# Performance work log

Measured on AMD Instinct MI355X. Metric: run time of the kernel, lower is better.

The kernel has to match this reference:

```python
import jax, jax.numpy as jnp
import numpy as np

B, N, NP, NS = 4, 8192, 2048, 32
CIN, COUT = 128, 256
RADIUS = 0.2
RELU_ALPHA = 0.2
BN_EPS = 1e-5


def setup_inputs() -> dict:
    key = jax.random.key(0)
    k1, k2, k3, k4, k5, k6, k7 = jax.random.split(key, 7)
    xyz = jax.random.uniform(k1, (B, N, 3), dtype=jnp.float32)          # points in unit cube
    feats = jax.random.normal(k2, (B, CIN, N), dtype=jnp.float32)
    conv_w = jax.random.normal(k3, (COUT, CIN), dtype=jnp.float32) * 0.05  # 1x1 conv kernel (bias off: bn=True)
    gamma = jax.random.uniform(k4, (COUT,), minval=0.5, maxval=1.5)
    beta = jax.random.normal(k5, (COUT,)) * 0.1
    rmean = jax.random.normal(k6, (COUT,)) * 0.1                        # BN running mean (eval mode)
    rvar = jax.random.uniform(k7, (COUT,), minval=0.5, maxval=1.5)      # BN running var
    return dict(xyz=xyz, feats=feats, conv_w=conv_w, gamma=gamma,
                beta=beta, rmean=rmean, rvar=rvar)


def _fps(pts):
    """Furthest point sampling. pts: [N,3] -> [NP] int32 indices. Starts at index 0 (CUDA kernel convention)."""
    mind0 = jnp.sum((pts - pts[0]) ** 2, axis=-1)  # [N]

    def step(mind, _):
        i = jnp.argmax(mind)
        mind = jnp.minimum(mind, jnp.sum((pts - pts[i]) ** 2, axis=-1))
        return mind, i.astype(jnp.int32)

    _, idxs = jax.lax.scan(step, mind0, None, length=NP - 1)
    return jnp.concatenate([jnp.zeros((1,), jnp.int32), idxs])


def reference(xyz, feats, conv_w, gamma, beta, rmean, rvar):
    # --- furthest point sampling + gather centroids ---
    fidx = jax.vmap(_fps)(xyz)                                   # [B,NP]
    new_xyz = jnp.take_along_axis(xyz, fidx[:, :, None], axis=1)  # [B,NP,3]

    # --- ball query: first NS point indices (in order) with dist^2 < r^2, pad with first hit ---
    d2 = jnp.sum((new_xyz[:, :, None, :] - xyz[:, None, :, :]) ** 2, axis=-1)  # [B,NP,N]
    mask = d2 < (RADIUS * RADIUS)
    key_ = jnp.where(mask, jnp.arange(N, dtype=jnp.float32), jnp.float32(N))
    neg, _ = jax.lax.top_k(-key_, NS)                            # NS smallest keys
    idx = (-neg).astype(jnp.int32)                               # [B,NP,NS], ascending index order
    first = idx[..., :1]
    fallback = jnp.where(first < N, first, 0)                    # empty ball -> index 0 (kernel default)
    idx = jnp.where(idx < N, idx, fallback)

    # --- grouping + max pool over neighbors ---
    gped = jax.vmap(lambda f, i: f[:, i])(feats, idx)            # [B,CIN,NP,NS]
    pooled = jnp.max(gped, axis=-1)                              # [B,CIN,NP]

    # --- 1x1 conv (no bias) + BatchNorm (eval) + LeakyReLU ---
    out = jnp.einsum('oc,bcn->bon', conv_w, pooled)              # [B,COUT,NP]
    inv = gamma / jnp.sqrt(rvar + BN_EPS)
    out = out * inv[None, :, None] + (beta - rmean * inv)[None, :, None]
    return jax.nn.leaky_relu(out, RELU_ALPHA)
```

## Files before the change

kernel.cpp:

```cpp
#include <hip/hip_runtime.h>
#include <cstdint>
#include <cstddef>

#define BB 4
#define NN 8192
#define NPP 2048
#define NSS 32
#define CINN 128
#define COUTT 256

template<int CTRL>
static __device__ __forceinline__ float dppf(float v){
  return __int_as_float(__builtin_amdgcn_update_dpp(0, __float_as_int(v), CTRL, 0xF, 0xF, true));
}
static __device__ __forceinline__ float wave_max63(float v){
  v = fmaxf(v, dppf<0xB1>(v));
  v = fmaxf(v, dppf<0x4E>(v));
  v = fmaxf(v, dppf<0x141>(v));
  v = fmaxf(v, dppf<0x140>(v));
  v = fmaxf(v, dppf<0x142>(v));
  v = fmaxf(v, dppf<0x143>(v));
  return v;
}
static __device__ __forceinline__ float red16_maxf(float v){
  v = fmaxf(v, dppf<0xB1>(v));
  v = fmaxf(v, dppf<0x4E>(v));
  v = fmaxf(v, dppf<0x141>(v));
  v = fmaxf(v, dppf<0x140>(v));
  return v;
}

__global__ __launch_bounds__(1024)
void k_pre(const float* __restrict__ xyz, const float* __restrict__ feats,
           const float* __restrict__ convw,
           int* __restrict__ fidx, float* __restrict__ featsT, float* __restrict__ wT)
{
  __shared__ union {
    struct {
      float  xs[NN];
      float  ys[NN];
      float  zs[NN];
      float2 slots[2][16];
    } fps;
    float tile[32][65];
  } sm;
  const int tid = threadIdx.x;
  const int blk = blockIdx.x;

  if (blk < BB) {
    const int b = blk;
    float* xs = sm.fps.xs;
    float* ys = sm.fps.ys;
    float* zs = sm.fps.zs;

    for (int n = tid; n < NN; n += 1024){
      const float* p = xyz + ((size_t)b*NN + n)*3;
      xs[n] = p[0]; ys[n] = p[1]; zs[n] = p[2];
    }
    __syncthreads();

    float px[8], py[8], pz[8], mind[8];
    const int base = tid*8;
    #pragma unroll
    for (int j=0;j<8;++j){
      px[j]=xs[base+j]; py[j]=ys[base+j]; pz[j]=zs[base+j];
      mind[j]=3.0e38f;
    }
    int cur = 0;
    if (tid == 0) fidx[b*NPP] = 0;
    const int lane = tid & 63;
    const int wid  = tid >> 6;

    for (int s = 1; s < NPP; ++s){
      const float cx = xs[cur], cy = ys[cur], cz = zs[cur];
      float bv = -1.0f; int bj = 0;
      #pragma unroll
      for (int j=0;j<8;++j){
        const float dx = px[j]-cx, dy = py[j]-cy, dz = pz[j]-cz;
        const float d2 = fmaf(dz,dz, fmaf(dy,dy, dx*dx));
        const float m  = fminf(mind[j], d2);
        mind[j] = m;
        const bool g = m > bv;
        bv = g ? m : bv;
        bj = g ? j : bj;
      }
      const int bi = base + bj;

      float wm = wave_max63(bv);
      wm = __int_as_float(__builtin_amdgcn_readlane(__float_as_int(wm), 63));
      const unsigned long long lm = __ballot(bv == wm);
      const int wl = (int)__builtin_ctzll(lm);
      const int wi = __builtin_amdgcn_readlane(bi, wl);

      const int par = s & 1;
      if (lane == 0) sm.fps.slots[par][wid] = make_float2(wm, __int_as_float(wi));
      __syncthreads();

      const float2 sv = sm.fps.slots[par][lane & 15];
      const int ci = __float_as_int(sv.y);
      const float gm = red16_maxf(sv.x);
      const unsigned long long bm = __ballot(sv.x == gm);
      const int ws = (int)__builtin_ctzll(bm);
      cur = __builtin_amdgcn_readlane(ci, ws);

      if (tid == 0) fidx[b*NPP + s] = cur;
    }
  } else if (blk < BB + 2048) {
    const int tb = blk - BB;
    const int b  = tb >> 9;
    const int t  = tb & 511;
    const int r0 = (t & 3) * 32;
    const int c0 = (t >> 2) * 64;
    const float* in = feats + (size_t)b*CINN*NN;
    float* outp = featsT + (size_t)b*NN*CINN;
    const int tx = tid & 63, ty = tid >> 6;
    #pragma unroll
    for (int u=0;u<2;++u) sm.tile[ty + 16*u][tx] = in[(size_t)(r0+ty+16*u)*NN + (c0+tx)];
    __syncthreads();
    const int tx2 = tid & 31, ty2 = tid >> 5;
    #pragma unroll
    for (int u=0;u<2;++u) outp[(size_t)(c0+ty2+32*u)*CINN + (r0+tx2)] = sm.tile[tx2][ty2+32*u];
  } else {
    const int t  = blk - BB - 2048;
    const int r0 = (t >> 1) * 32;
    const int c0 = (t & 1) * 64;
    const int tx = tid & 63, ty = tid >> 6;
    #pragma unroll
    for (int u=0;u<2;++u) sm.tile[ty+16*u][tx] = convw[(size_t)(r0+ty+16*u)*CINN + (c0+tx)];
    __syncthreads();
    const int tx2 = tid & 31, ty2 = tid >> 5;
    #pragma unroll
    for (int u=0;u<2;++u) wT[(size_t)(c0+ty2+32*u)*COUTT + (r0+tx2)] = sm.tile[tx2][ty2+32*u];
  }
}

__global__ __launch_bounds__(256)
void k_ball(const float* __restrict__ xyz, const int* __restrict__ fidx, int* __restrict__ idxb)
{
  const int lane = threadIdx.x & 63;
  const int gw = blockIdx.x*4 + (threadIdx.x >> 6);
  const int b = gw >> 11;
  const int qi = fidx[gw];
  const float R2F = (float)(0.2 * 0.2);
  const float* q = xyz + ((size_t)b*NN + qi)*3;
  const float qx = q[0], qy = q[1], qz = q[2];
  const float* Bp = xyz + (size_t)b*NN*3;
  int* outp = idxb + (size_t)gw*NSS;
  int cnt = 0, first = -1;
  for (int base0 = 0; base0 < NN; base0 += 256){
    float d2u[4];
    #pragma unroll
    for (int u=0;u<4;++u){
      const float* P = Bp + (size_t)(base0 + u*64 + lane)*3;
      const float dx = P[0]-qx, dy = P[1]-qy, dz = P[2]-qz;
      d2u[u] = fmaf(dz,dz, fmaf(dy,dy, dx*dx));
    }
    #pragma unroll
    for (int u=0;u<4;++u){
      const bool hit = d2u[u] < R2F;
      const unsigned long long m = __ballot(hit);
      if (first < 0 && m != 0ull) first = base0 + u*64 + (int)__builtin_ctzll(m);
      const int slot = cnt + (int)__popcll(m & ((1ull<<lane)-1ull));
      if (hit && slot < NSS) outp[slot] = base0 + u*64 + lane;
      cnt += (int)__popcll(m);
    }
    if (cnt >= NSS) break;
  }
  if (cnt < NSS){
    const int f = (first >= 0) ? first : 0;
    if (lane >= cnt && lane < NSS) outp[lane] = f;
  }
}

__global__ __launch_bounds__(256)
void k_pool(const float* __restrict__ featsT, const int* __restrict__ idxb, float* __restrict__ pooledC)
{
  __shared__ int lidx[256];
  const int tid = threadIdx.x;
  const int blk = blockIdx.x;
  lidx[tid] = idxb[(size_t)blk*256 + tid];
  __syncthreads();
  const int hw = tid >> 5, l = tid & 31;
  const int q = blk*8 + hw;
  const int b = q >> 11, p = q & (NPP-1);
  const float4* basep = (const float4*)(featsT + (size_t)b*NN*CINN);
  float4 m = make_float4(-3e38f,-3e38f,-3e38f,-3e38f);
  #pragma unroll 8
  for (int s=0;s<NSS;++s){
    const int i = lidx[hw*32 + s];
    const float4 v = basep[(size_t)i*32 + l];
    m.x = fmaxf(m.x, v.x); m.y = fmaxf(m.y, v.y);
    m.z = fmaxf(m.z, v.z); m.w = fmaxf(m.w, v.w);
  }
  float* oc = pooledC + ((size_t)b*CINN + l*4)*NPP + p;
  oc[0] = m.x; oc[NPP] = m.y; oc[2*(size_t)NPP] = m.z; oc[3*(size_t)NPP] = m.w;
}

__global__ __launch_bounds__(256)
void k_gemm(const float* __restrict__ pooledC, const float* __restrict__ wT,
            const float* __restrict__ gamma, const float* __restrict__ beta,
            const float* __restrict__ rmean, const float* __restrict__ rvar,
            float* __restrict__ out)
{
  const int o = threadIdx.x;
  const int blk = blockIdx.x;
  const int b = blk >> 7;
  const int p0 = (blk & 127) << 4;
  const float* pc = pooledC + (size_t)b*CINN*NPP + p0;
  float acc[16];
  #pragma unroll
  for (int i=0;i<16;++i) acc[i]=0.f;
  #pragma unroll 4
  for (int c=0;c<CINN;++c){
    const float wv = wT[c*COUTT + o];
    const float4* pr = (const float4*)(pc + (size_t)c*NPP);
    #pragma unroll
    for (int qq=0;qq<4;++qq){
      const float4 pv = pr[qq];
      acc[4*qq+0] = fmaf(wv, pv.x, acc[4*qq+0]);
      acc[4*qq+1] = fmaf(wv, pv.y, acc[4*qq+1]);
      acc[4*qq+2] = fmaf(wv, pv.z, acc[4*qq+2]);
      acc[4*qq+3] = fmaf(wv, pv.w, acc[4*qq+3]);
    }
  }
  const float inv = gamma[o] / sqrtf(rvar[o] + 1e-5f);
  const float sh  = beta[o] - rmean[o]*inv;
  float4* op = (float4*)(out + ((size_t)b*COUTT + o)*NPP + p0);
  #pragma unroll
  for (int qq=0;qq<4;++qq){
    float4 y;
    float t0 = fmaf(acc[4*qq+0], inv, sh);
    float t1 = fmaf(acc[4*qq+1], inv, sh);
    float t2 = fmaf(acc[4*qq+2], inv, sh);
    float t3 = fmaf(acc[4*qq+3], inv, sh);
    y.x = t0 >= 0.f ? t0 : 0.2f*t0;
    y.y = t1 >= 0.f ? t1 : 0.2f*t1;
    y.z = t2 >= 0.f ? t2 : 0.2f*t2;
    y.w = t3 >= 0.f ? t3 : 0.2f*t3;
    op[qq] = y;
  }
}

extern "C" void kernel_launch(void* const* d_in, const int* in_sizes, int n_in,
                              void* d_out, int out_size, void* d_ws, size_t ws_size,
                              hipStream_t stream)
{
  (void)in_sizes; (void)n_in; (void)out_size; (void)ws_size;
  const float* xyz   = (const float*)d_in[0];
  const float* feats = (const float*)d_in[1];
  const float* convw = (const float*)d_in[2];
  const float* gamma = (const float*)d_in[3];
  const float* beta  = (const float*)d_in[4];
  const float* rmean = (const float*)d_in[5];
  const float* rvar  = (const float*)d_in[6];
  float* out = (float*)d_out;

  char* ws = (char*)d_ws;
  float* featsT  = (float*)(ws);
  float* pooledC = (float*)(ws + 16777216);
  float* wT      = (float*)(ws + 16777216 + 4194304);
  int*   fidx    = (int*)  (ws + 16777216 + 4194304 + 131072);
  int*   idxb    = (int*)  (ws + 16777216 + 4194304 + 131072 + 32768);

  k_pre <<<dim3(BB + 2048 + 16), dim3(1024), 0, stream>>>(xyz, feats, convw, fidx, featsT, wT);
  k_ball<<<dim3(2048),           dim3(256),  0, stream>>>(xyz, fidx, idxb);
  k_pool<<<dim3(1024),           dim3(256),  0, stream>>>(featsT, idxb, pooledC);
  k_gemm<<<dim3(512),            dim3(256),  0, stream>>>(pooledC, wT, gamma, beta, rmean, rvar, out);
}
```

Measured before the change: 1.861 ms.

## Shrink FPS block to 256 threads with 32 points per thread

The furthest-point-sampling block now runs 256 threads, each holding 32 points in registers, instead of 1024 threads with 8 points each. This cuts the cross-wave reduction from 16 waves to 4, which makes the per-step barrier and slot exchange cheaper on this serial critical path. The per-thread scan is split into two independent argmax chains to add instruction-level parallelism. Each thread now does more serial distance work per step and uses more registers, and the transpose blocks are adjusted to loop over 8 rows per thread.

```diff
diff --git a/kernel.cpp b/kernel.cpp
--- a/kernel.cpp
+++ b/kernel.cpp
@@ -22,15 +22,13 @@
   v = fmaxf(v, dppf<0x143>(v));
   return v;
 }
-static __device__ __forceinline__ float red16_maxf(float v){
+static __device__ __forceinline__ float red4_maxf(float v){
   v = fmaxf(v, dppf<0xB1>(v));
   v = fmaxf(v, dppf<0x4E>(v));
-  v = fmaxf(v, dppf<0x141>(v));
-  v = fmaxf(v, dppf<0x140>(v));
   return v;
 }
 
-__global__ __launch_bounds__(1024)
+__global__ __launch_bounds__(256)
 void k_pre(const float* __restrict__ xyz, const float* __restrict__ feats,
            const float* __restrict__ convw,
            int* __restrict__ fidx, float* __restrict__ featsT, float* __restrict__ wT)
@@ -40,7 +38,7 @@
       float  xs[NN];
       float  ys[NN];
       float  zs[NN];
-      float2 slots[2][16];
+      float2 slots[2][4];
     } fps;
     float tile[32][65];
   } sm;
@@ -53,16 +51,16 @@
     float* ys = sm.fps.ys;
     float* zs = sm.fps.zs;
 
-    for (int n = tid; n < NN; n += 1024){
+    for (int n = tid; n < NN; n += 256){
       const float* p = xyz + ((size_t)b*NN + n)*3;
       xs[n] = p[0]; ys[n] = p[1]; zs[n] = p[2];
     }
     __syncthreads();
 
-    float px[8], py[8], pz[8], mind[8];
-    const int base = tid*8;
-    #pragma unroll
-    for (int j=0;j<8;++j){
+    float px[32], py[32], pz[32], mind[32];
+    const int base = tid*32;
+    #pragma unroll
+    for (int j=0;j<32;++j){
       px[j]=xs[base+j]; py[j]=ys[base+j]; pz[j]=zs[base+j];
       mind[j]=3.0e38f;
     }
@@ -73,18 +71,32 @@
 
     for (int s = 1; s < NPP; ++s){
       const float cx = xs[cur], cy = ys[cur], cz = zs[cur];
-      float bv = -1.0f; int bj = 0;
+      float bvA = -1.0f, bvB = -1.0f; int bjA = 0, bjB = 16;
       #pragma unroll
-      for (int j=0;j<8;++j){
-        const float dx = px[j]-cx, dy = py[j]-cy, dz = pz[j]-cz;
-        const float d2 = fmaf(dz,dz, fmaf(dy,dy, dx*dx));
-        const float m  = fminf(mind[j], d2);
-        mind[j] = m;
-        const bool g = m > bv;
-        bv = g ? m : bv;
-        bj = g ? j : bj;
+      for (int j=0;j<16;++j){
+        {
+          const float dx = px[j]-cx, dy = py[j]-cy, dz = pz[j]-cz;
+          const float d2 = fmaf(dz,dz, fmaf(dy,dy, dx*dx));
+          const float m  = fminf(mind[j], d2);
+          mind[j] = m;
+          const bool g = m > bvA;
+          bvA = g ? m : bvA;
+          bjA = g ? j : bjA;
+        }
+        {
+          const int j2 = j + 16;
+          const float dx = px[j2]-cx, dy = py[j2]-cy, dz = pz[j2]-cz;
+          const float d2 = fmaf(dz,dz, fmaf(dy,dy, dx*dx));
+          const float m  = fminf(mind[j2], d2);
+          mind[j2] = m;
+          const bool g = m > bvB;
+          bvB = g ? m : bvB;
+          bjB = g ? j2 : bjB;
+        }
       }
-      const int bi = base + bj;
+      const bool gB = bvB > bvA;
+      const float bv = gB ? bvB : bvA;
+      const int   bi = base + (gB ? bjB : bjA);
 
       float wm = wave_max63(bv);
       wm = __int_as_float(__builtin_amdgcn_readlane(__float_as_int(wm), 63));
@@ -96,9 +108,9 @@
       if (lane == 0) sm.fps.slots[par][wid] = make_float2(wm, __int_as_float(wi));
       __syncthreads();
 
-      const float2 sv = sm.fps.slots[par][lane & 15];
+      const float2 sv = sm.fps.slots[par][lane & 3];
       const int ci = __float_as_int(sv.y);
-      const float gm = red16_maxf(sv.x);
+      const float gm = red4_maxf(sv.x);
       const unsigned long long bm = __ballot(sv.x == gm);
       const int ws = (int)__builtin_ctzll(bm);
       cur = __builtin_amdgcn_readlane(ci, ws);
@@ -115,22 +127,22 @@
     float* outp = featsT + (size_t)b*NN*CINN;
     const int tx = tid & 63, ty = tid >> 6;
     #pragma unroll
-    for (int u=0;u<2;++u) sm.tile[ty + 16*u][tx] = in[(size_t)(r0+ty+16*u)*NN + (c0+tx)];
+    for (int u=0;u<8;++u) sm.tile[ty + 4*u][tx] = in[(size_t)(r0+ty+4*u)*NN + (c0+tx)];
     __syncthreads();
     const int tx2 = tid & 31, ty2 = tid >> 5;
     #pragma unroll
-    for (int u=0;u<2;++u) outp[(size_t)(c0+ty2+32*u)*CINN + (r0+tx2)] = sm.tile[tx2][ty2+32*u];
+    for (int u=0;u<8;++u) outp[(size_t)(c0+ty2+8*u)*CINN + (r0+tx2)] = sm.tile[tx2][ty2+8*u];
   } else {
     const int t  = blk - BB - 2048;
     const int r0 = (t >> 1) * 32;
     const int c0 = (t & 1) * 64;
     const int tx = tid & 63, ty = tid >> 6;
     #pragma unroll
-    for (int u=0;u<2;++u) sm.tile[ty+16*u][tx] = convw[(size_t)(r0+ty+16*u)*CINN + (c0+tx)];
+    for (int u=0;u<8;++u) sm.tile[ty+4*u][tx] = convw[(size_t)(r0+ty+4*u)*CINN + (c0+tx)];
     __syncthreads();
     const int tx2 = tid & 31, ty2 = tid >> 5;
     #pragma unroll
-    for (int u=0;u<2;++u) wT[(size_t)(c0+ty2+32*u)*COUTT + (r0+tx2)] = sm.tile[tx2][ty2+32*u];
+    for (int u=0;u<8;++u) wT[(size_t)(c0+ty2+8*u)*COUTT + (r0+tx2)] = sm.tile[tx2][ty2+8*u];
   }
 }
 
@@ -262,8 +274,8 @@
   int*   fidx    = (int*)  (ws + 16777216 + 4194304 + 131072);
   int*   idxb    = (int*)  (ws + 16777216 + 4194304 + 131072 + 32768);
 
-  k_pre <<<dim3(BB + 2048 + 16), dim3(1024), 0, stream>>>(xyz, feats, convw, fidx, featsT, wT);
-  k_ball<<<dim3(2048),           dim3(256),  0, stream>>>(xyz, fidx, idxb);
-  k_pool<<<dim3(1024),           dim3(256),  0, stream>>>(featsT, idxb, pooledC);
-  k_gemm<<<dim3(512),            dim3(256),  0, stream>>>(pooledC, wT, gamma, beta, rmean, rvar, out);
-}
+  k_pre <<<dim3(BB + 2048 + 16), dim3(256), 0, stream>>>(xyz, feats, convw, fidx, featsT, wT);
+  k_ball<<<dim3(2048),           dim3(256), 0, stream>>>(xyz, fidx, idxb);
+  k_pool<<<dim3(1024),           dim3(256), 0, stream>>>(featsT, idxb, pooledC);
+  k_gemm<<<dim3(512),            dim3(256), 0, stream>>>(pooledC, wT, gamma, beta, rmean, rvar, out);
+}
```

After: 1.970 ms. 1.06x slower.

## Use shared atomicMax argmax in FPS, halve block size, fuse ball query with pooling

Applied to the files above, without the earlier changes.

The FPS loop now packs the per-wave max distance and its point index into a 64-bit key and combines waves with a shared-memory atomicMax. This replaces the second-level slot reduction, and the code rotates four cells so each one can be cleared ahead of reuse. Blocks shrink to 512 threads, each holding 16 points, and the coordinates are stored as float4 in LDS. The ball query and max-pool kernels are fused so neighbour indices stay in LDS instead of a global round trip. The risks are more serial work per thread in the latency-bound FPS loop and contention on the shared atomics.

```diff
diff --git a/kernel.cpp b/kernel.cpp
--- a/kernel.cpp
+++ b/kernel.cpp
@@ -22,25 +22,16 @@
   v = fmaxf(v, dppf<0x143>(v));
   return v;
 }
-static __device__ __forceinline__ float red16_maxf(float v){
-  v = fmaxf(v, dppf<0xB1>(v));
-  v = fmaxf(v, dppf<0x4E>(v));
-  v = fmaxf(v, dppf<0x141>(v));
-  v = fmaxf(v, dppf<0x140>(v));
-  return v;
-}
-
-__global__ __launch_bounds__(1024)
+
+__global__ __launch_bounds__(512)
 void k_pre(const float* __restrict__ xyz, const float* __restrict__ feats,
            const float* __restrict__ convw,
            int* __restrict__ fidx, float* __restrict__ featsT, float* __restrict__ wT)
 {
   __shared__ union {
     struct {
-      float  xs[NN];
-      float  ys[NN];
-      float  zs[NN];
-      float2 slots[2][16];
+      float4 xyzw[NN];
+      unsigned long long cell[4];
     } fps;
     float tile[32][65];
   } sm;
@@ -49,33 +40,34 @@
 
   if (blk < BB) {
     const int b = blk;
-    float* xs = sm.fps.xs;
-    float* ys = sm.fps.ys;
-    float* zs = sm.fps.zs;
-
-    for (int n = tid; n < NN; n += 1024){
+    float4* P4 = sm.fps.xyzw;
+    for (int n = tid; n < NN; n += 512){
       const float* p = xyz + ((size_t)b*NN + n)*3;
-      xs[n] = p[0]; ys[n] = p[1]; zs[n] = p[2];
+      P4[n] = make_float4(p[0], p[1], p[2], 0.f);
+    }
+    if (tid == 0){
+      sm.fps.cell[0] = 0ull; sm.fps.cell[1] = 0ull;
+      sm.fps.cell[2] = 0ull; sm.fps.cell[3] = 0ull;
+      fidx[b*NPP] = 0;
     }
     __syncthreads();
 
-    float px[8], py[8], pz[8], mind[8];
-    const int base = tid*8;
-    #pragma unroll
-    for (int j=0;j<8;++j){
-      px[j]=xs[base+j]; py[j]=ys[base+j]; pz[j]=zs[base+j];
+    float px[16], py[16], pz[16], mind[16];
+    const int base = tid*16;
+    #pragma unroll
+    for (int j=0;j<16;++j){
+      const float4 p4 = P4[base+j];
+      px[j]=p4.x; py[j]=p4.y; pz[j]=p4.z;
       mind[j]=3.0e38f;
     }
-    int cur = 0;
-    if (tid == 0) fidx[b*NPP] = 0;
     const int lane = tid & 63;
-    const int wid  = tid >> 6;
+    const float4 c0 = P4[0];
+    float cx=c0.x, cy=c0.y, cz=c0.z;
 
     for (int s = 1; s < NPP; ++s){
-      const float cx = xs[cur], cy = ys[cur], cz = zs[cur];
       float bv = -1.0f; int bj = 0;
       #pragma unroll
-      for (int j=0;j<8;++j){
+      for (int j=0;j<16;++j){
         const float dx = px[j]-cx, dy = py[j]-cy, dz = pz[j]-cz;
         const float d2 = fmaf(dz,dz, fmaf(dy,dy, dx*dx));
         const float m  = fminf(mind[j], d2);
@@ -86,23 +78,20 @@
       }
       const int bi = base + bj;
 
+      const unsigned long long key =
+        ((unsigned long long)__float_as_uint(bv) << 16) | (unsigned)(8191 - bi);
+
       float wm = wave_max63(bv);
       wm = __int_as_float(__builtin_amdgcn_readlane(__float_as_int(wm), 63));
-      const unsigned long long lm = __ballot(bv == wm);
-      const int wl = (int)__builtin_ctzll(lm);
-      const int wi = __builtin_amdgcn_readlane(bi, wl);
-
-      const int par = s & 1;
-      if (lane == 0) sm.fps.slots[par][wid] = make_float2(wm, __int_as_float(wi));
+      const int cidx = s & 3;
+      if (bv == wm) atomicMax(&sm.fps.cell[cidx], key);
       __syncthreads();
 
-      const float2 sv = sm.fps.slots[par][lane & 15];
-      const int ci = __float_as_int(sv.y);
-      const float gm = red16_maxf(sv.x);
-      const unsigned long long bm = __ballot(sv.x == gm);
-      const int ws = (int)__builtin_ctzll(bm);
-      cur = __builtin_amdgcn_readlane(ci, ws);
-
+      const unsigned long long k = sm.fps.cell[cidx];
+      const int cur = 8191 - (int)(k & 0xFFFFull);
+      if (lane == 0) sm.fps.cell[(s + 2) & 3] = 0ull;
+      const float4 w4 = P4[cur];
+      cx = w4.x; cy = w4.y; cz = w4.z;
       if (tid == 0) fidx[b*NPP + s] = cur;
     }
   } else if (blk < BB + 2048) {
@@ -115,85 +104,89 @@
     float* outp = featsT + (size_t)b*NN*CINN;
     const int tx = tid & 63, ty = tid >> 6;
     #pragma unroll
-    for (int u=0;u<2;++u) sm.tile[ty + 16*u][tx] = in[(size_t)(r0+ty+16*u)*NN + (c0+tx)];
+    for (int u=0;u<4;++u) sm.tile[ty + 8*u][tx] = in[(size_t)(r0+ty+8*u)*NN + (c0+tx)];
     __syncthreads();
     const int tx2 = tid & 31, ty2 = tid >> 5;
     #pragma unroll
-    for (int u=0;u<2;++u) outp[(size_t)(c0+ty2+32*u)*CINN + (r0+tx2)] = sm.tile[tx2][ty2+32*u];
+    for (int u=0;u<4;++u) outp[(size_t)(c0+ty2+16*u)*CINN + (r0+tx2)] = sm.tile[tx2][ty2+16*u];
   } else {
     const int t  = blk - BB - 2048;
     const int r0 = (t >> 1) * 32;
     const int c0 = (t & 1) * 64;
     const int tx = tid & 63, ty = tid >> 6;
     #pragma unroll
-    for (int u=0;u<2;++u) sm.tile[ty+16*u][tx] = convw[(size_t)(r0+ty+16*u)*CINN + (c0+tx)];
+    for (int u=0;u<4;++u) sm.tile[ty+8*u][tx] = convw[(size_t)(r0+ty+8*u)*CINN + (c0+tx)];
     __syncthreads();
     const int tx2 = tid & 31, ty2 = tid >> 5;
     #pragma unroll
-    for (int u=0;u<2;++u) wT[(size_t)(c0+ty2+32*u)*COUTT + (r0+tx2)] = sm.tile[tx2][ty2+32*u];
+    for (int u=0;u<4;++u) wT[(size_t)(c0+ty2+16*u)*COUTT + (r0+tx2)] = sm.tile[tx2][ty2+16*u];
   }
 }
 
 __global__ __launch_bounds__(256)
-void k_ball(const float* __restrict__ xyz, const int* __restrict__ fidx, int* __restrict__ idxb)
-{
-  const int lane = threadIdx.x & 63;
-  const int gw = blockIdx.x*4 + (threadIdx.x >> 6);
+void k_ballpool(const float* __restrict__ xyz, const int* __restrict__ fidx,
+                const float* __restrict__ featsT, float* __restrict__ pooledC)
+{
+  __shared__ int lidx[4*NSS];
+  const int tid = threadIdx.x;
+  const int lane = tid & 63;
+  const int w = tid >> 6;
+  const int gw = blockIdx.x*4 + w;
   const int b = gw >> 11;
-  const int qi = fidx[gw];
-  const float R2F = (float)(0.2 * 0.2);
-  const float* q = xyz + ((size_t)b*NN + qi)*3;
-  const float qx = q[0], qy = q[1], qz = q[2];
-  const float* Bp = xyz + (size_t)b*NN*3;
-  int* outp = idxb + (size_t)gw*NSS;
-  int cnt = 0, first = -1;
-  for (int base0 = 0; base0 < NN; base0 += 256){
-    float d2u[4];
-    #pragma unroll
-    for (int u=0;u<4;++u){
-      const float* P = Bp + (size_t)(base0 + u*64 + lane)*3;
-      const float dx = P[0]-qx, dy = P[1]-qy, dz = P[2]-qz;
-      d2u[u] = fmaf(dz,dz, fmaf(dy,dy, dx*dx));
-    }
-    #pragma unroll
-    for (int u=0;u<4;++u){
-      const bool hit = d2u[u] < R2F;
-      const unsigned long long m = __ballot(hit);
-      if (first < 0 && m != 0ull) first = base0 + u*64 + (int)__builtin_ctzll(m);
-      const int slot = cnt + (int)__popcll(m & ((1ull<<lane)-1ull));
-      if (hit && slot < NSS) outp[slot] = base0 + u*64 + lane;
-      cnt += (int)__popcll(m);
-    }
-    if (cnt >= NSS) break;
-  }
-  if (cnt < NSS){
-    const int f = (first >= 0) ? first : 0;
-    if (lane >= cnt && lane < NSS) outp[lane] = f;
-  }
-}
-
-__global__ __launch_bounds__(256)
-void k_pool(const float* __restrict__ featsT, const int* __restrict__ idxb, float* __restrict__ pooledC)
-{
-  __shared__ int lidx[256];
-  const int tid = threadIdx.x;
-  const int blk = blockIdx.x;
-  lidx[tid] = idxb[(size_t)blk*256 + tid];
+
+  {
+    const int qi = fidx[gw];
+    const float R2F = (float)(0.2 * 0.2);
+    const float* q = xyz + ((size_t)b*NN + qi)*3;
+    const float qx = q[0], qy = q[1], qz = q[2];
+    const float* Bp = xyz + (size_t)b*NN*3;
+    int cnt = 0, first = -1;
+    for (int base0 = 0; base0 < NN; base0 += 256){
+      float d2u[4];
+      #pragma unroll
+      for (int u=0;u<4;++u){
+        const float* P = Bp + (size_t)(base0 + u*64 + lane)*3;
+        const float dx = P[0]-qx, dy = P[1]-qy, dz = P[2]-qz;
+        d2u[u] = fmaf(dz,dz, fmaf(dy,dy, dx*dx));
+      }
+      #pragma unroll
+      for (int u=0;u<4;++u){
+        const bool hit = d2u[u] < R2F;
+        const unsigned long long m = __ballot(hit);
+        if (first < 0 && m != 0ull) first = base0 + u*64 + (int)__builtin_ctzll(m);
+        const int slot = cnt + (int)__popcll(m & ((1ull<<lane)-1ull));
+        if (hit && slot < NSS) lidx[w*NSS + slot] = base0 + u*64 + lane;
+        cnt += (int)__popcll(m);
+      }
+      if (cnt >= NSS) break;
+    }
+    if (cnt < NSS){
+      const int f = (first >= 0) ? first : 0;
+      if (lane >= cnt && lane < NSS) lidx[w*NSS + lane] = f;
+    }
+  }
   __syncthreads();
-  const int hw = tid >> 5, l = tid & 31;
-  const int q = blk*8 + hw;
-  const int b = q >> 11, p = q & (NPP-1);
+
+  const int c4 = lane & 31;
+  const int sh = lane >> 5;
   const float4* basep = (const float4*)(featsT + (size_t)b*NN*CINN);
   float4 m = make_float4(-3e38f,-3e38f,-3e38f,-3e38f);
   #pragma unroll 8
-  for (int s=0;s<NSS;++s){
-    const int i = lidx[hw*32 + s];
-    const float4 v = basep[(size_t)i*32 + l];
+  for (int t=0;t<16;++t){
+    const int i = lidx[w*NSS + 2*t + sh];
+    const float4 v = basep[(size_t)i*32 + c4];
     m.x = fmaxf(m.x, v.x); m.y = fmaxf(m.y, v.y);
     m.z = fmaxf(m.z, v.z); m.w = fmaxf(m.w, v.w);
   }
-  float* oc = pooledC + ((size_t)b*CINN + l*4)*NPP + p;
-  oc[0] = m.x; oc[NPP] = m.y; oc[2*(size_t)NPP] = m.z; oc[3*(size_t)NPP] = m.w;
+  m.x = fmaxf(m.x, __shfl_xor(m.x, 32, 64));
+  m.y = fmaxf(m.y, __shfl_xor(m.y, 32, 64));
+  m.z = fmaxf(m.z, __shfl_xor(m.z, 32, 64));
+  m.w = fmaxf(m.w, __shfl_xor(m.w, 32, 64));
+  if (sh == 0){
+    const int p = gw & (NPP-1);
+    float* oc = pooledC + ((size_t)b*CINN + c4*4)*NPP + p;
+    oc[0] = m.x; oc[NPP] = m.y; oc[2*(size_t)NPP] = m.z; oc[3*(size_t)NPP] = m.w;
+  }
 }
 
 __global__ __launch_bounds__(256)
@@ -260,10 +253,8 @@
   float* pooledC = (float*)(ws + 16777216);
   float* wT      = (float*)(ws + 16777216 + 4194304);
   int*   fidx    = (int*)  (ws + 16777216 + 4194304 + 131072);
-  int*   idxb    = (int*)  (ws + 16777216 + 4194304 + 131072 + 32768);
-
-  k_pre <<<dim3(BB + 2048 + 16), dim3(1024), 0, stream>>>(xyz, feats, convw, fidx, featsT, wT);
-  k_ball<<<dim3(2048),           dim3(256),  0, stream>>>(xyz, fidx, idxb);
-  k_pool<<<dim3(1024),           dim3(256),  0, stream>>>(featsT, idxb, pooledC);
-  k_gemm<<<dim3(512),            dim3(256),  0, stream>>>(pooledC, wT, gamma, beta, rmean, rvar, out);
-}
+
+  k_pre     <<<dim3(BB + 2048 + 16), dim3(512), 0, stream>>>(xyz, feats, convw, fidx, featsT, wT);
+  k_ballpool<<<dim3(2048),           dim3(256), 0, stream>>>(xyz, fidx, featsT, pooledC);
+  k_gemm    <<<dim3(512),            dim3(256), 0, stream>>>(pooledC, wT, gamma, beta, rmean, rvar, out);
+}
```

New measurement: 1.666 ms. 10.5% less time.
